# Kernel tuning notes

Measured on AMD Instinct MI355X. Metric: run time of the kernel, lower is better.

## Reference

```python
import jax, jax.numpy as jnp
import numpy as np

# CLEVR-scale dims
B, N, DF, DE, DV, H, NC, QV, L = 128, 36, 512, 256, 512, 256, 28, 2000, 5


def _lin(key, fan_in, fan_out):
    k1, _ = jax.random.split(key)
    w = jax.random.normal(k1, (fan_in, fan_out), jnp.float32) * np.sqrt(2.0 / fan_in)  # kaiming
    b = jnp.zeros((fan_out,), jnp.float32)
    return w, b


def setup_inputs() -> dict:
    key = jax.random.key(0)
    ks = jax.random.split(key, 12)
    node_feats = jax.random.normal(ks[0], (B, N, DF), jnp.float32)
    edge_feats = jax.random.normal(ks[1], (B, N, N, DE), jnp.float32)
    programs = jax.random.randint(ks[2], (B, L), 0, 10)
    program_inputs = jax.random.randint(ks[3], (B, L), 0, QV)
    W_n1, b_n1 = _lin(ks[4], DF, H)
    W_n2, b_n2 = _lin(ks[5], H, DV)
    W_e1, b_e1 = _lin(ks[6], DE, H)
    W_e2, b_e2 = _lin(ks[7], H, DV)
    W_q, b_q = _lin(ks[8], DV, DV)
    W_c1, b_c1 = _lin(ks[9], DV, H)
    W_c2, b_c2 = _lin(ks[10], H, NC)
    word_emb = jax.random.normal(ks[11], (QV, DV), jnp.float32) / np.sqrt(DV)
    return dict(node_feats=node_feats, edge_feats=edge_feats,
                W_n1=W_n1, b_n1=b_n1, W_n2=W_n2, b_n2=b_n2,
                W_e1=W_e1, b_e1=b_e1, W_e2=W_e2, b_e2=b_e2,
                W_q=W_q, b_q=b_q, W_c1=W_c1, b_c1=b_c1,
                W_c2=W_c2, b_c2=b_c2, word_emb=word_emb,
                programs=programs, program_inputs=program_inputs)


def _mlp(x, W1, b1, W2, b2):
    return jax.nn.relu(x @ W1 + b1) @ W2 + b2


def reference(node_feats, edge_feats, W_n1, b_n1, W_n2, b_n2,
              W_e1, b_e1, W_e2, b_e2, W_q, b_q,
              W_c1, b_c1, W_c2, b_c2, word_emb,
              programs, program_inputs):
    # Fixed representative program (executed in reverse order like the torch code):
    # scene -> filter -> relate -> filter -> query -> classifier
    del programs
    scale = 1.0 / np.sqrt(DV)
    nf = _mlp(node_feats, W_n1, b_n1, W_n2, b_n2)      # [B,N,DV]  map_node_feat_to_v
    ef = _mlp(edge_feats, W_e1, b_e1, W_e2, b_e2)      # [B,N,N,DV] map_edge_feat_to_v
    q = word_emb[program_inputs]                        # [B,L,DV]  word_embedding lookup
    # scene: attention of ones over nodes
    attn = jnp.ones(nf.shape[:2], nf.dtype)             # [B,N]
    # filter (AttentionModule): gate node attention by query-node similarity
    attn = attn * jax.nn.sigmoid(jnp.einsum('bnd,bd->bn', nf, q[:, 3]) * scale)
    # relate (RelateModule): transfer attention along query-weighted edges
    weit = jax.nn.sigmoid(jnp.einsum('bijd,bd->bij', ef, q[:, 2]) * scale)  # [B,N,N]
    attn = jnp.clip(jnp.einsum('bi,bij->bj', attn, weit), 0.0, 1.0)
    # filter again
    attn = attn * jax.nn.sigmoid(jnp.einsum('bnd,bd->bn', nf, q[:, 1]) * scale)
    # query (QueryModule): attention-pooled node feature gated by query, projected
    attn_n = attn / (attn.sum(-1, keepdims=True) + 1e-8)
    pooled = jnp.einsum('bn,bnd->bd', attn_n, nf)        # [B,DV]
    out = jax.nn.relu((pooled * q[:, 0]) @ W_q + b_q)    # [B,DV]
    # classifier
    return jax.nn.relu(out @ W_c1 + b_c1) @ W_c2 + b_c2  # [B,NC]
```

## Files before the change

### kernel.cpp

```cpp
#include <hip/hip_runtime.h>
#include <math.h>

#define BB 128
#define NN 36
#define DF 512
#define DE 256
#define DV 512
#define HH 256
#define NCC 28
#define LQ 5
#define NE 1296
#define SCALE 0.04419417382415922f

#define ETILES 10368
#define EBLOCKS 256
#define EWAVES 2048
#define NODE_PAIRS 144

typedef __bf16 bf16_8 __attribute__((ext_vector_type(8)));
typedef float  f32_4  __attribute__((ext_vector_type(4)));

__device__ __forceinline__ float sigmoidf_(float x){ return 1.0f/(1.0f + expf(-x)); }
__device__ __forceinline__ float reluf_(float x){ return x > 0.f ? x : 0.f; }

__device__ __forceinline__ bf16_8 cvt8(f32_4 f0, f32_4 f1){
    bf16_8 v;
    #pragma unroll
    for (int i=0;i<4;i++){ v[i] = (__bf16)f0[i]; v[i+4] = (__bf16)f1[i]; }
    return v;
}
__device__ __forceinline__ void split8(f32_4 f0, f32_4 f1, bf16_8& h, bf16_8& l){
    #pragma unroll
    for (int i=0;i<4;i++){
        __bf16 hi = (__bf16)f0[i];
        h[i] = hi; l[i] = (__bf16)(f0[i] - (float)hi);
        __bf16 hi2 = (__bf16)f1[i];
        h[i+4] = hi2; l[i+4] = (__bf16)(f1[i] - (float)hi2);
    }
}

__device__ __forceinline__ void async_copy16(const float* g, float* lds_base){
    __builtin_amdgcn_global_load_lds(
        (const __attribute__((address_space(1))) void*)g,
        (__attribute__((address_space(3))) void*)lds_base, 16, 0, 0);
}

#define XROW 516

__global__ __launch_bounds__(256) void k_setup(
    const float* __restrict__ W_n1, const float* __restrict__ W_n2,
    const float* __restrict__ W_e1,
    const float* __restrict__ word_emb, const int* __restrict__ program_inputs,
    const float* __restrict__ W_e2, const float* __restrict__ b_e2,
    __bf16* __restrict__ Pn1h, __bf16* __restrict__ Pn1l,
    __bf16* __restrict__ Pn2h, __bf16* __restrict__ Pn2l,
    __bf16* __restrict__ Peh,
    float* __restrict__ qws, float* __restrict__ ve, float* __restrict__ se)
{
    int bid = blockIdx.x;
    if (bid < 160){
        const float* W; __bf16 *Ph, *Pl; int N, base, realN;
        if (bid < 64)       { W=W_n1; Ph=Pn1h; Pl=Pn1l; N=256; base=0;   realN=256; }
        else if (bid < 128) { W=W_n2; Ph=Pn2h; Pl=Pn2l; N=512; base=64;  realN=512; }
        else                { W=W_e1; Ph=Peh;  Pl=nullptr; N=256; base=128; realN=256; }
        int g = (bid-base)*256 + threadIdx.x;
        int lane = g & 63, slot = g >> 6;
        int NT = N >> 4;
        int nt = slot % NT, kt = slot / NT;
        int krow = kt*32 + (lane>>4)*8, ncol = nt*16 + (lane&15);
        #pragma unroll
        for (int j=0;j<8;j++){
            float w = (ncol < realN) ? W[(size_t)(krow+j)*realN + ncol] : 0.f;
            __bf16 hi = (__bf16)w;
            Ph[(size_t)g*8+j] = hi;
            if (Pl) Pl[(size_t)g*8+j] = (__bf16)(w - (float)hi);
        }
    } else {
        int b = bid - 160, t = threadIdx.x, wv = t>>6, lane = t&63;
        int idx[4];
        #pragma unroll
        for (int k=0;k<4;k++) idx[k] = program_inputs[b*LQ + k];
        #pragma unroll
        for (int k=0;k<4;k++){
            qws[((size_t)(b*4+k))*DV + t]       = word_emb[(size_t)idx[k]*DV + t];
            qws[((size_t)(b*4+k))*DV + t + 256] = word_emb[(size_t)idx[k]*DV + t + 256];
        }
        const float* q2p = word_emb + (size_t)idx[2]*DV + lane*8;
        f32_4 qa = *(const f32_4*)q2p, qb = *(const f32_4*)(q2p+4);
        for (int i=0;i<64;i++){
            int h = wv*64 + i;
            const float* wr = W_e2 + (size_t)h*DV + lane*8;
            f32_4 a = *(const f32_4*)wr, c = *(const f32_4*)(wr+4);
            float p = a[0]*qa[0] + a[1]*qa[1] + a[2]*qa[2] + a[3]*qa[3]
                    + c[0]*qb[0] + c[1]*qb[1] + c[2]*qb[2] + c[3]*qb[3];
            #pragma unroll
            for (int off=32; off; off>>=1) p += __shfl_xor(p, off, 64);
            if (lane==0) ve[b*HH + h] = p;
        }
        float pp = b_e2[t]*word_emb[(size_t)idx[2]*DV + t]
                 + b_e2[t+256]*word_emb[(size_t)idx[2]*DV + t + 256];
        __shared__ float red[4];
        #pragma unroll
        for (int off=32; off; off>>=1) pp += __shfl_down(pp, off, 64);
        if ((t&63)==0) red[t>>6] = pp;
        __syncthreads();
        if (t==0) se[b] = red[0]+red[1]+red[2]+red[3];
    }
}

__device__ __forceinline__ void node_body(
    int nb, char* smem, int t,
    const float* __restrict__ X,
    const __bf16* __restrict__ W1h, const __bf16* __restrict__ W1l,
    const float* __restrict__ b1,
    const __bf16* __restrict__ W2h, const __bf16* __restrict__ W2l,
    const float* __restrict__ b2,
    float* __restrict__ nf)
{
    float* xs  = (float*)smem;
    __bf16* hh = (__bf16*)(smem + 33024);
    __bf16* hl = (__bf16*)(smem + 41216);
    int r0 = nb*16, wv = t>>6, lane = t&63;
    int m = lane&15, kc = lane>>4;
    int q = lane>>4, c = lane&15;

    #pragma unroll
    for (int r=0;r<4;r++){
        int row = wv*4 + r;
        const float* src = X + (size_t)(r0+row)*DF + lane*4;
        async_copy16(src,       &xs[row*XROW]);
        async_copy16(src + 256, &xs[row*XROW + 256]);
    }
    __syncthreads();

    f32_4 zero = {0.f,0.f,0.f,0.f};
    f32_4 acc1[4];
    #pragma unroll
    for (int nt=0;nt<4;nt++) acc1[nt] = zero;
    for (int kt=0; kt<16; kt++){
        const float* ap = &xs[m*XROW + kt*32 + kc*8];
        f32_4 f0 = *(const f32_4*)ap;
        f32_4 f1 = *(const f32_4*)(ap+4);
        bf16_8 ah, al;
        split8(f0, f1, ah, al);
        #pragma unroll
        for (int nt=0;nt<4;nt++){
            size_t bo = ((size_t)(kt*16 + wv*4+nt)*64 + lane)*8;
            bf16_8 bh = *(const bf16_8*)(W1h + bo);
            bf16_8 bl = *(const bf16_8*)(W1l + bo);
            acc1[nt] = __builtin_amdgcn_mfma_f32_16x16x32_bf16(ah, bh, acc1[nt], 0,0,0);
            acc1[nt] = __builtin_amdgcn_mfma_f32_16x16x32_bf16(al, bh, acc1[nt], 0,0,0);
            acc1[nt] = __builtin_amdgcn_mfma_f32_16x16x32_bf16(ah, bl, acc1[nt], 0,0,0);
        }
    }
    #pragma unroll
    for (int nt=0;nt<4;nt++){
        int col = wv*64 + nt*16 + c;
        float bias = b1[col];
        int kt2 = col>>5, j2 = col&7;
        int lbase = ((col&31)>>3)*16;
        #pragma unroll
        for (int r=0;r<4;r++){
            int row = q*4 + r;
            float v = reluf_(acc1[nt][r] + bias);
            __bf16 hi = (__bf16)v;
            int off = (kt2*64 + lbase + row)*8 + j2;
            hh[off] = hi;
            hl[off] = (__bf16)(v - (float)hi);
        }
    }
    __syncthreads();

    f32_4 acc2[8];
    #pragma unroll
    for (int nt=0;nt<8;nt++) acc2[nt] = zero;
    for (int kt=0; kt<8; kt++){
        bf16_8 ah = *(const bf16_8*)&hh[(kt*64+lane)*8];
        bf16_8 al = *(const bf16_8*)&hl[(kt*64+lane)*8];
        #pragma unroll
        for (int nt=0;nt<8;nt++){
            size_t bo = ((size_t)(kt*32 + wv*8+nt)*64 + lane)*8;
            bf16_8 bh = *(const bf16_8*)(W2h + bo);
            bf16_8 bl = *(const bf16_8*)(W2l + bo);
            acc2[nt] = __builtin_amdgcn_mfma_f32_16x16x32_bf16(ah, bh, acc2[nt], 0,0,0);
            acc2[nt] = __builtin_amdgcn_mfma_f32_16x16x32_bf16(al, bh, acc2[nt], 0,0,0);
            acc2[nt] = __builtin_amdgcn_mfma_f32_16x16x32_bf16(ah, bl, acc2[nt], 0,0,0);
        }
    }
    #pragma unroll
    for (int nt=0;nt<8;nt++){
        int col = wv*128 + nt*16 + c;
        float bias = b2[col];
        #pragma unroll
        for (int r=0;r<4;r++){
            int row = q*4 + r;
            nf[(size_t)(r0+row)*DV + col] = acc2[nt][r] + bias;
        }
    }
}

__device__ __forceinline__ void edge_body(
    char* smem,
    const float* __restrict__ E, const __bf16* __restrict__ Wp,
    const float* __restrict__ b_e1, const float* __restrict__ ve,
    const float* __restrict__ se, float* __restrict__ weit)
{
    __bf16* wlds = (__bf16*)smem;
    int t = threadIdx.x, wv = t>>6, lane = t&63;
    int m = lane&15, kc = lane>>4;

    #pragma unroll
    for (int i=0;i<16;i++){
        int off = (wv*16 + i) << 10;
        async_copy16((const float*)((const char*)Wp + off) + lane*4,
                     (float*)((char*)wlds + off));
    }
    __syncthreads();

    for (int tile = blockIdx.x*8 + wv; tile < ETILES; tile += EWAVES){
        int b = tile/81, tt = tile - b*81;
        int e0 = tt*16;
        const float* Ea = E + ((size_t)b*NE + e0 + m)*DE + kc*8;
        float seb = se[b];
        float s0=0.f, s1=0.f, s2=0.f, s3=0.f;

        #pragma unroll 1
        for (int half=0; half<2; half++){
            f32_4 zero = {0.f,0.f,0.f,0.f};
            f32_4 acc[8];
            #pragma unroll
            for (int nt=0;nt<8;nt++) acc[nt] = zero;

            f32_4 c0 = *(const f32_4*)Ea;
            f32_4 c1 = *(const f32_4*)(Ea + 4);
            #pragma unroll 1
            for (int kt=0;kt<8;kt++){
                int kn = (kt+1)&7;
                f32_4 n0 = *(const f32_4*)(Ea + kn*32);
                f32_4 n1 = *(const f32_4*)(Ea + kn*32 + 4);
                bf16_8 af = cvt8(c0, c1);
                const __bf16* wb = wlds + ((size_t)(kt*16 + half*8)*64 + lane)*8;
                #pragma unroll
                for (int nt=0;nt<8;nt++){
                    bf16_8 bfrag = *(const bf16_8*)(wb + (size_t)nt*512);
                    acc[nt] = __builtin_amdgcn_mfma_f32_16x16x32_bf16(af, bfrag, acc[nt], 0,0,0);
                }
                c0 = n0; c1 = n1;
            }
            #pragma unroll
            for (int nt=0;nt<8;nt++){
                int h = (half*8 + nt)*16 + m;
                float bev = b_e1[h];
                float vev = ve[b*HH + h];
                s0 = fmaf(reluf_(acc[nt][0] + bev), vev, s0);
                s1 = fmaf(reluf_(acc[nt][1] + bev), vev, s1);
                s2 = fmaf(reluf_(acc[nt][2] + bev), vev, s2);
                s3 = fmaf(reluf_(acc[nt][3] + bev), vev, s3);
            }
        }

        #pragma unroll
        for (int off=1; off<16; off<<=1){
            s0 += __shfl_xor(s0, off, 64);
            s1 += __shfl_xor(s1, off, 64);
            s2 += __shfl_xor(s2, off, 64);
            s3 += __shfl_xor(s3, off, 64);
        }
        if (m == 0){
            f32_4 o;
            o[0] = sigmoidf_((s0 + seb)*SCALE);
            o[1] = sigmoidf_((s1 + seb)*SCALE);
            o[2] = sigmoidf_((s2 + seb)*SCALE);
            o[3] = sigmoidf_((s3 + seb)*SCALE);
            *(f32_4*)&weit[(size_t)b*NE + e0 + kc*4] = o;
        }
    }
}

__global__ __launch_bounds__(512, 1) void k_main(
    const float* __restrict__ E, const __bf16* __restrict__ Wp,
    const float* __restrict__ b_e1, const float* __restrict__ ve,
    const float* __restrict__ se, float* __restrict__ weit,
    const float* __restrict__ X,
    const __bf16* __restrict__ W1h, const __bf16* __restrict__ W1l,
    const float* __restrict__ b1,
    const __bf16* __restrict__ W2h, const __bf16* __restrict__ W2l,
    const float* __restrict__ b2,
    float* __restrict__ nf)
{
    __shared__ __align__(16) char smem[131072];
    int bx = blockIdx.x;
    if (bx < EBLOCKS){
        edge_body(smem, E, Wp, b_e1, ve, se, weit);
    } else {
        int sub = threadIdx.x >> 8;
        int nb = (bx - EBLOCKS)*2 + sub;
        node_body(nb, smem + sub*49408, threadIdx.x & 255,
                  X, W1h, W1l, b1, W2h, W2l, b2, nf);
    }
}

__global__ __launch_bounds__(512) void k_attnhead(
    const float* __restrict__ nf, const float* __restrict__ qws,
    const float* __restrict__ weit,
    const float* __restrict__ Wq,  const float* __restrict__ bq,
    const float* __restrict__ Wc1, const float* __restrict__ bc1,
    const float* __restrict__ Wc2, const float* __restrict__ bc2,
    float* __restrict__ out)
{
    int b = blockIdx.x, t = threadIdx.x;
    int wv = t>>6, lane = t&63;
    __shared__ float a1[NN], a3[NN];
    __shared__ float xsh[DV];
    __shared__ float osh[DV];
    __shared__ float hsh[HH];
    __shared__ float denom;
    const float* nfb = nf + (size_t)b*NN*DV;
    const float* q0 = qws + ((size_t)(b*4+0))*DV;
    const float* q1 = qws + ((size_t)(b*4+1))*DV;
    const float* q3 = qws + ((size_t)(b*4+3))*DV;

    for (int i=wv; i<NN; i+=8){
        const float* row = nfb + (size_t)i*DV + lane*8;
        const float* qq  = q3 + lane*8;
        f32_4 x0 = *(const f32_4*)row, x1 = *(const f32_4*)(row+4);
        f32_4 y0 = *(const f32_4*)qq,  y1 = *(const f32_4*)(qq+4);
        float p = x0[0]*y0[0] + x0[1]*y0[1] + x0[2]*y0[2] + x0[3]*y0[3]
                + x1[0]*y1[0] + x1[1]*y1[1] + x1[2]*y1[2] + x1[3]*y1[3];
        #pragma unroll
        for (int off=32; off; off>>=1) p += __shfl_xor(p, off, 64);
        if (lane==0) a1[i] = sigmoidf_(p*SCALE);
    }
    __syncthreads();
    __shared__ float a2[NN];
    if (t < NN){
        const float* wrow = weit + (size_t)b*NE;
        float s = 0.f;
        #pragma unroll
        for (int i=0;i<NN;i++) s = fmaf(a1[i], wrow[i*NN + t], s);
        a2[t] = fminf(fmaxf(s, 0.f), 1.f);
    }
    __syncthreads();
    for (int i=wv; i<NN; i+=8){
        const float* row = nfb + (size_t)i*DV + lane*8;
        const float* qq  = q1 + lane*8;
        f32_4 x0 = *(const f32_4*)row, x1 = *(const f32_4*)(row+4);
        f32_4 y0 = *(const f32_4*)qq,  y1 = *(const f32_4*)(qq+4);
        float p = x0[0]*y0[0] + x0[1]*y0[1] + x0[2]*y0[2] + x0[3]*y0[3]
                + x1[0]*y1[0] + x1[1]*y1[1] + x1[2]*y1[2] + x1[3]*y1[3];
        #pragma unroll
        for (int off=32; off; off>>=1) p += __shfl_xor(p, off, 64);
        if (lane==0) a3[i] = a2[i]*sigmoidf_(p*SCALE);
    }
    __syncthreads();
    if (t==0){
        float s = 0.f;
        for (int i=0;i<NN;i++) s += a3[i];
        denom = 1.f/(s + 1e-8f);
    }
    __syncthreads();
    if (t < NN) a3[t] *= denom;
    __syncthreads();

    {
        float p = 0.f;
        #pragma unroll 4
        for (int i=0;i<NN;i++) p = fmaf(a3[i], nfb[(size_t)i*DV + t], p);
        xsh[t] = p * q0[t];
    }
    __syncthreads();

    {
        float acc = bq[t];
        #pragma unroll 8
        for (int k=0;k<DV;k++) acc = fmaf(xsh[k], Wq[(size_t)k*DV + t], acc);
        osh[t] = reluf_(acc);
    }
    __syncthreads();

    if (t < HH){
        float acc = bc1[t];
        #pragma unroll 8
        for (int k=0;k<DV;k++) acc = fmaf(osh[k], Wc1[(size_t)k*HH + t], acc);
        hsh[t] = reluf_(acc);
    }
    __syncthreads();

    if (t < NCC){
        float acc = bc2[t];
        #pragma unroll 8
        for (int k=0;k<HH;k++) acc = fmaf(hsh[k], Wc2[(size_t)k*NCC + t], acc);
        out[(size_t)b*NCC + t] = acc;
    }
}

extern "C" void kernel_launch(void* const* d_in, const int* in_sizes, int n_in,
                              void* d_out, int out_size, void* d_ws, size_t ws_size,
                              hipStream_t stream)
{
    const float* node_feats = (const float*)d_in[0];
    const float* edge_feats = (const float*)d_in[1];
    const float* W_n1 = (const float*)d_in[2];
    const float* b_n1 = (const float*)d_in[3];
    const float* W_n2 = (const float*)d_in[4];
    const float* b_n2 = (const float*)d_in[5];
    const float* W_e1 = (const float*)d_in[6];
    const float* b_e1 = (const float*)d_in[7];
    const float* W_e2 = (const float*)d_in[8];
    const float* b_e2 = (const float*)d_in[9];
    const float* W_q  = (const float*)d_in[10];
    const float* b_q  = (const float*)d_in[11];
    const float* W_c1 = (const float*)d_in[12];
    const float* b_c1 = (const float*)d_in[13];
    const float* W_c2 = (const float*)d_in[14];
    const float* b_c2 = (const float*)d_in[15];
    const float* word_emb = (const float*)d_in[16];
    const int* program_inputs = (const int*)d_in[18];

    char* ws = (char*)d_ws;
    float* qws  = (float*)ws; ws += (size_t)BB*4*DV*4;
    float* ve   = (float*)ws; ws += (size_t)BB*HH*4;
    float* se   = (float*)ws; ws += 512;
    __bf16* Pn1h = (__bf16*)ws; ws += (size_t)DF*HH*2;
    __bf16* Pn1l = (__bf16*)ws; ws += (size_t)DF*HH*2;
    __bf16* Pn2h = (__bf16*)ws; ws += (size_t)HH*DV*2;
    __bf16* Pn2l = (__bf16*)ws; ws += (size_t)HH*DV*2;
    __bf16* Peh  = (__bf16*)ws; ws += (size_t)DE*HH*2;
    float* nf   = (float*)ws; ws += (size_t)BB*NN*DV*4;
    float* weit = (float*)ws; ws += (size_t)BB*NE*4;

    k_setup<<<288, 256, 0, stream>>>(W_n1, W_n2, W_e1,
                                     word_emb, program_inputs, W_e2, b_e2,
                                     Pn1h, Pn1l, Pn2h, Pn2l, Peh, qws, ve, se);
    k_main<<<EBLOCKS + NODE_PAIRS, 512, 0, stream>>>(
        edge_feats, Peh, b_e1, ve, se, weit,
        node_feats, Pn1h, Pn1l, b_n1, Pn2h, Pn2l, b_n2, nf);
    k_attnhead<<<BB, 512, 0, stream>>>(nf, qws, weit,
                                       W_q, b_q, W_c1, b_c1, W_c2, b_c2,
                                       (float*)d_out);
}
```

Before: 455.4 us.

## Fuse setup, main and head kernels into one cooperative persistent kernel

Merges the three launches into a single cooperative kernel of 256 blocks that uses grid-wide syncs between the weight-packing/query setup, the node/edge MLP phase and the attention head. Edge tiles are now handed out dynamically through an atomic counter, so blocks that finish their node work can pick up edge tiles, replacing the fixed strided assignment. The edge loop also computes all 16 output column tiles in one pass instead of two halves, which avoids re-reading the edge inputs at the cost of more accumulator registers. The aim is to remove launch gaps and imbalance between node and edge blocks. The risks are grid-sync overhead, register pressure from 16 accumulators, and a serial head phase that uses only 128 of the blocks.

```diff
diff --git a/kernel.cpp b/kernel.cpp
--- a/kernel.cpp
+++ b/kernel.cpp
@@ -1,5 +1,8 @@
 #include <hip/hip_runtime.h>
+#include <hip/hip_cooperative_groups.h>
 #include <math.h>
+
+namespace cg = cooperative_groups;
 
 #define BB 128
 #define NN 36
@@ -13,8 +16,7 @@
 #define SCALE 0.04419417382415922f
 
 #define ETILES 10368
-#define EBLOCKS 256
-#define EWAVES 2048
+#define GRID 256
 #define NODE_PAIRS 144
 
 typedef __bf16 bf16_8 __attribute__((ext_vector_type(8)));
@@ -46,67 +48,6 @@
 }
 
 #define XROW 516
-
-__global__ __launch_bounds__(256) void k_setup(
-    const float* __restrict__ W_n1, const float* __restrict__ W_n2,
-    const float* __restrict__ W_e1,
-    const float* __restrict__ word_emb, const int* __restrict__ program_inputs,
-    const float* __restrict__ W_e2, const float* __restrict__ b_e2,
-    __bf16* __restrict__ Pn1h, __bf16* __restrict__ Pn1l,
-    __bf16* __restrict__ Pn2h, __bf16* __restrict__ Pn2l,
-    __bf16* __restrict__ Peh,
-    float* __restrict__ qws, float* __restrict__ ve, float* __restrict__ se)
-{
-    int bid = blockIdx.x;
-    if (bid < 160){
-        const float* W; __bf16 *Ph, *Pl; int N, base, realN;
-        if (bid < 64)       { W=W_n1; Ph=Pn1h; Pl=Pn1l; N=256; base=0;   realN=256; }
-        else if (bid < 128) { W=W_n2; Ph=Pn2h; Pl=Pn2l; N=512; base=64;  realN=512; }
-        else                { W=W_e1; Ph=Peh;  Pl=nullptr; N=256; base=128; realN=256; }
-        int g = (bid-base)*256 + threadIdx.x;
-        int lane = g & 63, slot = g >> 6;
-        int NT = N >> 4;
-        int nt = slot % NT, kt = slot / NT;
-        int krow = kt*32 + (lane>>4)*8, ncol = nt*16 + (lane&15);
-        #pragma unroll
-        for (int j=0;j<8;j++){
-            float w = (ncol < realN) ? W[(size_t)(krow+j)*realN + ncol] : 0.f;
-            __bf16 hi = (__bf16)w;
-            Ph[(size_t)g*8+j] = hi;
-            if (Pl) Pl[(size_t)g*8+j] = (__bf16)(w - (float)hi);
-        }
-    } else {
-        int b = bid - 160, t = threadIdx.x, wv = t>>6, lane = t&63;
-        int idx[4];
-        #pragma unroll
-        for (int k=0;k<4;k++) idx[k] = program_inputs[b*LQ + k];
-        #pragma unroll
-        for (int k=0;k<4;k++){
-            qws[((size_t)(b*4+k))*DV + t]       = word_emb[(size_t)idx[k]*DV + t];
-            qws[((size_t)(b*4+k))*DV + t + 256] = word_emb[(size_t)idx[k]*DV + t + 256];
-        }
-        const float* q2p = word_emb + (size_t)idx[2]*DV + lane*8;
-        f32_4 qa = *(const f32_4*)q2p, qb = *(const f32_4*)(q2p+4);
-        for (int i=0;i<64;i++){
-            int h = wv*64 + i;
-            const float* wr = W_e2 + (size_t)h*DV + lane*8;
-            f32_4 a = *(const f32_4*)wr, c = *(const f32_4*)(wr+4);
-            float p = a[0]*qa[0] + a[1]*qa[1] + a[2]*qa[2] + a[3]*qa[3]
-                    + c[0]*qb[0] + c[1]*qb[1] + c[2]*qb[2] + c[3]*qb[3];
-            #pragma unroll
-            for (int off=32; off; off>>=1) p += __shfl_xor(p, off, 64);
-            if (lane==0) ve[b*HH + h] = p;
-        }
-        float pp = b_e2[t]*word_emb[(size_t)idx[2]*DV + t]
-                 + b_e2[t+256]*word_emb[(size_t)idx[2]*DV + t + 256];
-        __shared__ float red[4];
-        #pragma unroll
-        for (int off=32; off; off>>=1) pp += __shfl_down(pp, off, 64);
-        if ((t&63)==0) red[t>>6] = pp;
-        __syncthreads();
-        if (t==0) se[b] = red[0]+red[1]+red[2]+red[3];
-    }
-}
 
 __device__ __forceinline__ void node_body(
     int nb, char* smem, int t,
@@ -203,7 +144,8 @@
     char* smem,
     const float* __restrict__ E, const __bf16* __restrict__ Wp,
     const float* __restrict__ b_e1, const float* __restrict__ ve,
-    const float* __restrict__ se, float* __restrict__ weit)
+    const float* __restrict__ se, float* __restrict__ weit,
+    int* __restrict__ ctr)
 {
     __bf16* wlds = (__bf16*)smem;
     int t = threadIdx.x, wv = t>>6, lane = t&63;
@@ -217,48 +159,50 @@
     }
     __syncthreads();
 
-    for (int tile = blockIdx.x*8 + wv; tile < ETILES; tile += EWAVES){
+    for(;;){
+        int tile;
+        if (lane == 0) tile = atomicAdd(ctr, 1);
+        tile = __shfl(tile, 0, 64);
+        if (tile >= ETILES) break;
+
         int b = tile/81, tt = tile - b*81;
         int e0 = tt*16;
         const float* Ea = E + ((size_t)b*NE + e0 + m)*DE + kc*8;
         float seb = se[b];
+
+        f32_4 zero = {0.f,0.f,0.f,0.f};
+        f32_4 acc[16];
+        #pragma unroll
+        for (int nt=0;nt<16;nt++) acc[nt] = zero;
+
+        f32_4 c0 = *(const f32_4*)Ea;
+        f32_4 c1 = *(const f32_4*)(Ea + 4);
+        #pragma unroll 1
+        for (int kt=0;kt<8;kt++){
+            int kn = (kt+1)&7;
+            f32_4 n0 = *(const f32_4*)(Ea + kn*32);
+            f32_4 n1 = *(const f32_4*)(Ea + kn*32 + 4);
+            bf16_8 af = cvt8(c0, c1);
+            const __bf16* wb = wlds + ((size_t)(kt*16)*64 + lane)*8;
+            #pragma unroll
+            for (int nt=0;nt<16;nt++){
+                bf16_8 bfrag = *(const bf16_8*)(wb + (size_t)nt*512);
+                acc[nt] = __builtin_amdgcn_mfma_f32_16x16x32_bf16(af, bfrag, acc[nt], 0,0,0);
+            }
+            c0 = n0; c1 = n1;
+        }
+
         float s0=0.f, s1=0.f, s2=0.f, s3=0.f;
-
-        #pragma unroll 1
-        for (int half=0; half<2; half++){
-            f32_4 zero = {0.f,0.f,0.f,0.f};
-            f32_4 acc[8];
-            #pragma unroll
-            for (int nt=0;nt<8;nt++) acc[nt] = zero;
-
-            f32_4 c0 = *(const f32_4*)Ea;
-            f32_4 c1 = *(const f32_4*)(Ea + 4);
-            #pragma unroll 1
-            for (int kt=0;kt<8;kt++){
-                int kn = (kt+1)&7;
-                f32_4 n0 = *(const f32_4*)(Ea + kn*32);
-                f32_4 n1 = *(const f32_4*)(Ea + kn*32 + 4);
-                bf16_8 af = cvt8(c0, c1);
-                const __bf16* wb = wlds + ((size_t)(kt*16 + half*8)*64 + lane)*8;
-                #pragma unroll
-                for (int nt=0;nt<8;nt++){
-                    bf16_8 bfrag = *(const bf16_8*)(wb + (size_t)nt*512);
-                    acc[nt] = __builtin_amdgcn_mfma_f32_16x16x32_bf16(af, bfrag, acc[nt], 0,0,0);
-                }
-                c0 = n0; c1 = n1;
-            }
-            #pragma unroll
-            for (int nt=0;nt<8;nt++){
-                int h = (half*8 + nt)*16 + m;
-                float bev = b_e1[h];
-                float vev = ve[b*HH + h];
-                s0 = fmaf(reluf_(acc[nt][0] + bev), vev, s0);
-                s1 = fmaf(reluf_(acc[nt][1] + bev), vev, s1);
-                s2 = fmaf(reluf_(acc[nt][2] + bev), vev, s2);
-                s3 = fmaf(reluf_(acc[nt][3] + bev), vev, s3);
-            }
-        }
-
+        #pragma unroll
+        for (int nt=0;nt<16;nt++){
+            int h = nt*16 + m;
+            float bev = b_e1[h];
+            float vev = ve[b*HH + h];
+            s0 = fmaf(reluf_(acc[nt][0] + bev), vev, s0);
+            s1 = fmaf(reluf_(acc[nt][1] + bev), vev, s1);
+            s2 = fmaf(reluf_(acc[nt][2] + bev), vev, s2);
+            s3 = fmaf(reluf_(acc[nt][3] + bev), vev, s3);
+        }
         #pragma unroll
         for (int off=1; off<16; off<<=1){
             s0 += __shfl_xor(s0, off, 64);
@@ -277,30 +221,8 @@
     }
 }
 
-__global__ __launch_bounds__(512, 1) void k_main(
-    const float* __restrict__ E, const __bf16* __restrict__ Wp,
-    const float* __restrict__ b_e1, const float* __restrict__ ve,
-    const float* __restrict__ se, float* __restrict__ weit,
-    const float* __restrict__ X,
-    const __bf16* __restrict__ W1h, const __bf16* __restrict__ W1l,
-    const float* __restrict__ b1,
-    const __bf16* __restrict__ W2h, const __bf16* __restrict__ W2l,
-    const float* __restrict__ b2,
-    float* __restrict__ nf)
-{
-    __shared__ __align__(16) char smem[131072];
-    int bx = blockIdx.x;
-    if (bx < EBLOCKS){
-        edge_body(smem, E, Wp, b_e1, ve, se, weit);
-    } else {
-        int sub = threadIdx.x >> 8;
-        int nb = (bx - EBLOCKS)*2 + sub;
-        node_body(nb, smem + sub*49408, threadIdx.x & 255,
-                  X, W1h, W1l, b1, W2h, W2l, b2, nf);
-    }
-}
-
-__global__ __launch_bounds__(512) void k_attnhead(
+__device__ __forceinline__ void attnhead_body(
+    char* smem, int b,
     const float* __restrict__ nf, const float* __restrict__ qws,
     const float* __restrict__ weit,
     const float* __restrict__ Wq,  const float* __restrict__ bq,
@@ -308,13 +230,15 @@
     const float* __restrict__ Wc2, const float* __restrict__ bc2,
     float* __restrict__ out)
 {
-    int b = blockIdx.x, t = threadIdx.x;
+    float* a1  = (float*)smem;
+    float* a2  = a1 + 64;
+    float* a3  = a2 + 64;
+    float* xsh = a3 + 64;
+    float* osh = xsh + 512;
+    float* hsh = osh + 512;
+    float* dn  = hsh + 256;
+    int t = threadIdx.x;
     int wv = t>>6, lane = t&63;
-    __shared__ float a1[NN], a3[NN];
-    __shared__ float xsh[DV];
-    __shared__ float osh[DV];
-    __shared__ float hsh[HH];
-    __shared__ float denom;
     const float* nfb = nf + (size_t)b*NN*DV;
     const float* q0 = qws + ((size_t)(b*4+0))*DV;
     const float* q1 = qws + ((size_t)(b*4+1))*DV;
@@ -332,7 +256,6 @@
         if (lane==0) a1[i] = sigmoidf_(p*SCALE);
     }
     __syncthreads();
-    __shared__ float a2[NN];
     if (t < NN){
         const float* wrow = weit + (size_t)b*NE;
         float s = 0.f;
@@ -356,10 +279,10 @@
     if (t==0){
         float s = 0.f;
         for (int i=0;i<NN;i++) s += a3[i];
-        denom = 1.f/(s + 1e-8f);
-    }
-    __syncthreads();
-    if (t < NN) a3[t] *= denom;
+        dn[0] = 1.f/(s + 1e-8f);
+    }
+    __syncthreads();
+    if (t < NN) a3[t] *= dn[0];
     __syncthreads();
 
     {
@@ -391,6 +314,102 @@
         #pragma unroll 8
         for (int k=0;k<HH;k++) acc = fmaf(hsh[k], Wc2[(size_t)k*NCC + t], acc);
         out[(size_t)b*NCC + t] = acc;
+    }
+}
+
+__global__ __launch_bounds__(512, 1) void k_all(
+    const float* __restrict__ E, const float* __restrict__ X,
+    const float* __restrict__ W_n1, const float* __restrict__ b_n1,
+    const float* __restrict__ W_n2, const float* __restrict__ b_n2,
+    const float* __restrict__ W_e1, const float* __restrict__ b_e1,
+    const float* __restrict__ W_e2, const float* __restrict__ b_e2,
+    const float* __restrict__ W_q,  const float* __restrict__ b_q,
+    const float* __restrict__ W_c1, const float* __restrict__ b_c1,
+    const float* __restrict__ W_c2, const float* __restrict__ b_c2,
+    const float* __restrict__ word_emb, const int* __restrict__ program_inputs,
+    __bf16* __restrict__ Pn1h, __bf16* __restrict__ Pn1l,
+    __bf16* __restrict__ Pn2h, __bf16* __restrict__ Pn2l,
+    __bf16* __restrict__ Peh,
+    float* __restrict__ qws, float* __restrict__ ve, float* __restrict__ se,
+    float* __restrict__ nf, float* __restrict__ weit,
+    int* __restrict__ ctr, float* __restrict__ out)
+{
+    cg::grid_group grid = cg::this_grid();
+    __shared__ __align__(16) char smem[131072];
+    int bx = blockIdx.x;
+
+    {
+        int sub = threadIdx.x >> 8, t = threadIdx.x & 255;
+        int vbid = bx*2 + sub;
+        if (vbid < 160){
+            const float* W; __bf16 *Ph, *Pl; int N, base, realN;
+            if (vbid < 64)       { W=W_n1; Ph=Pn1h; Pl=Pn1l; N=256; base=0;   realN=256; }
+            else if (vbid < 128) { W=W_n2; Ph=Pn2h; Pl=Pn2l; N=512; base=64;  realN=512; }
+            else                 { W=W_e1; Ph=Peh;  Pl=nullptr; N=256; base=128; realN=256; }
+            int g = (vbid-base)*256 + t;
+            int lane = g & 63, slot = g >> 6;
+            int NT = N >> 4;
+            int nt = slot % NT, kt = slot / NT;
+            int krow = kt*32 + (lane>>4)*8, ncol = nt*16 + (lane&15);
+            #pragma unroll
+            for (int j=0;j<8;j++){
+                float w = (ncol < realN) ? W[(size_t)(krow+j)*realN + ncol] : 0.f;
+                __bf16 hi = (__bf16)w;
+                Ph[(size_t)g*8+j] = hi;
+                if (Pl) Pl[(size_t)g*8+j] = (__bf16)(w - (float)hi);
+            }
+        } else if (vbid < 288){
+            __shared__ float red[2][4];
+            int b = vbid - 160, wv = t>>6, lane = t&63;
+            int idx[4];
+            #pragma unroll
+            for (int k=0;k<4;k++) idx[k] = program_inputs[b*LQ + k];
+            #pragma unroll
+            for (int k=0;k<4;k++){
+                qws[((size_t)(b*4+k))*DV + t]       = word_emb[(size_t)idx[k]*DV + t];
+                qws[((size_t)(b*4+k))*DV + t + 256] = word_emb[(size_t)idx[k]*DV + t + 256];
+            }
+            const float* q2p = word_emb + (size_t)idx[2]*DV + lane*8;
+            f32_4 qa = *(const f32_4*)q2p, qb = *(const f32_4*)(q2p+4);
+            for (int i=0;i<64;i++){
+                int h = wv*64 + i;
+                const float* wr = W_e2 + (size_t)h*DV + lane*8;
+                f32_4 a = *(const f32_4*)wr, c = *(const f32_4*)(wr+4);
+                float p = a[0]*qa[0] + a[1]*qa[1] + a[2]*qa[2] + a[3]*qa[3]
+                        + c[0]*qb[0] + c[1]*qb[1] + c[2]*qb[2] + c[3]*qb[3];
+                #pragma unroll
+                for (int off=32; off; off>>=1) p += __shfl_xor(p, off, 64);
+                if (lane==0) ve[b*HH + h] = p;
+            }
+            float pp = b_e2[t]*word_emb[(size_t)idx[2]*DV + t]
+                     + b_e2[t+256]*word_emb[(size_t)idx[2]*DV + t + 256];
+            #pragma unroll
+            for (int off=32; off; off>>=1) pp += __shfl_down(pp, off, 64);
+            if ((t&63)==0) red[sub][t>>6] = pp;
+            __syncthreads();
+            if (t==0) se[b] = red[sub][0]+red[sub][1]+red[sub][2]+red[sub][3];
+        }
+        if (bx == GRID-1 && threadIdx.x == 0) *ctr = 0;
+    }
+    __threadfence();
+    grid.sync();
+
+    {
+        if (bx < NODE_PAIRS){
+            int sub = threadIdx.x >> 8;
+            int nb = bx*2 + sub;
+            node_body(nb, smem + sub*49408, threadIdx.x & 255,
+                      X, Pn1h, Pn1l, b_n1, Pn2h, Pn2l, b_n2, nf);
+            __syncthreads();
+        }
+        edge_body(smem, E, Peh, b_e1, ve, se, weit, ctr);
+    }
+    __threadfence();
+    grid.sync();
+
+    if (bx < BB){
+        attnhead_body(smem, bx, nf, qws, weit,
+                      W_q, b_q, W_c1, b_c1, W_c2, b_c2, out);
     }
 }
 
@@ -428,14 +447,19 @@
     __bf16* Peh  = (__bf16*)ws; ws += (size_t)DE*HH*2;
     float* nf   = (float*)ws; ws += (size_t)BB*NN*DV*4;
     float* weit = (float*)ws; ws += (size_t)BB*NE*4;
-
-    k_setup<<<288, 256, 0, stream>>>(W_n1, W_n2, W_e1,
-                                     word_emb, program_inputs, W_e2, b_e2,
-                                     Pn1h, Pn1l, Pn2h, Pn2l, Peh, qws, ve, se);
-    k_main<<<EBLOCKS + NODE_PAIRS, 512, 0, stream>>>(
-        edge_feats, Peh, b_e1, ve, se, weit,
-        node_feats, Pn1h, Pn1l, b_n1, Pn2h, Pn2l, b_n2, nf);
-    k_attnhead<<<BB, 512, 0, stream>>>(nf, qws, weit,
-                                       W_q, b_q, W_c1, b_c1, W_c2, b_c2,
-                                       (float*)d_out);
-}
+    int*   ctr  = (int*)ws;   ws += 256;
+    float* out_f = (float*)d_out;
+
+    void* args[] = {
+        (void*)&edge_feats, (void*)&node_feats,
+        (void*)&W_n1, (void*)&b_n1, (void*)&W_n2, (void*)&b_n2,
+        (void*)&W_e1, (void*)&b_e1, (void*)&W_e2, (void*)&b_e2,
+        (void*)&W_q,  (void*)&b_q,  (void*)&W_c1, (void*)&b_c1,
+        (void*)&W_c2, (void*)&b_c2, (void*)&word_emb, (void*)&program_inputs,
+        (void*)&Pn1h, (void*)&Pn1l, (void*)&Pn2h, (void*)&Pn2l, (void*)&Peh,
+        (void*)&qws, (void*)&ve, (void*)&se, (void*)&nf, (void*)&weit,
+        (void*)&ctr, (void*)&out_f
+    };
+    hipLaunchCooperativeKernel((const void*)k_all, dim3(GRID), dim3(512),
+                               args, 0, stream);
+}
```

After: 678.5 us. 49.0% more time.
